# Kernel tuning notes

Hardware: AMD Instinct MI355X
Metric: run time of the kernel (lower is better)

The kernel has to match this reference:

```python
import jax, jax.numpy as jnp
import numpy as np

B = 512      # graphs per batch
NPG = 62     # nodes (electrodes) per graph
N = B * NPG  # total nodes per band
F_IN = 5     # node features
H = 8        # attention heads
C = 3        # num_classes (GATConv out channels, concat=False)
DEG = 16     # avg degree
EG = NPG * DEG
E = B * EG   # edges per band
NB = 5       # bands: delta, alpha, beta, theta, gamma
DE_DIM = 930 # 310*3


def setup_inputs() -> dict:
    key = jax.random.key(0)
    ks = jax.random.split(key, 24)
    x_bands = jax.random.normal(ks[0], (NB, N, F_IN), dtype=jnp.float32)
    # within-graph random edges: node ids in [g*62, g*62+62)
    base = (jnp.arange(B, dtype=jnp.int32) * NPG)[None, :, None]
    src = jax.random.randint(ks[1], (NB, B, EG), 0, NPG, dtype=jnp.int32) + base
    dst = jax.random.randint(ks[2], (NB, B, EG), 0, NPG, dtype=jnp.int32) + base
    edge_index_bands = jnp.stack([src.reshape(NB, E), dst.reshape(NB, E)], axis=1)  # [NB,2,E]
    batch = jnp.repeat(jnp.arange(B, dtype=jnp.int32), NPG)  # [N]
    de = jax.random.normal(ks[3], (B, NPG, 5, 3), dtype=jnp.float32)
    s = 0.3
    params = dict(
        bn_gamma=jnp.ones((NB, F_IN), jnp.float32),
        bn_beta=jnp.zeros((NB, F_IN), jnp.float32),
        W=jax.random.normal(ks[4], (NB, F_IN, H * C)) * s,
        att_src=jax.random.normal(ks[5], (NB, H, C)) * s,
        att_dst=jax.random.normal(ks[6], (NB, H, C)) * s,
        gat_bias=jax.random.normal(ks[7], (NB, C)) * 0.01,
        fg_W=jax.random.normal(ks[8], (NB * C, 64)) * s,
        fg_b=jnp.zeros((64,), jnp.float32),
        ln_g=jnp.ones((DE_DIM,), jnp.float32),
        ln_b=jnp.zeros((DE_DIM,), jnp.float32),
        q_W=jax.random.normal(ks[9], (DE_DIM, 64)) * 0.03,
        q_b=jnp.zeros((64,), jnp.float32),
        k_W=jax.random.normal(ks[10], (DE_DIM, 64)) * 0.03,
        k_b=jnp.zeros((64,), jnp.float32),
        v_W=jax.random.normal(ks[11], (DE_DIM, 64)) * 0.03,
        v_b=jnp.zeros((64,), jnp.float32),
        fa_W=jax.random.normal(ks[12], (128, C)) * s,
        fa_b=jnp.zeros((C,), jnp.float32),
    )
    return dict(x_bands=x_bands, edge_index_bands=edge_index_bands, batch=batch, de=de, **params)


def _gat_band(x, ei, g, b, Wb, a_src, a_dst, bias, batch):
    # BatchNorm1d (training-mode batch stats), eps=1e-5
    mu = x.mean(0)
    var = x.var(0)
    xn = (x - mu) * jax.lax.rsqrt(var + 1e-5) * g + b
    # GATConv(F_IN -> C, heads=H, concat=False) with self-loops
    xt = (xn @ Wb).reshape(N, H, C)                       # [N,H,C]
    al_s = (xt * a_src).sum(-1)                           # [N,H]
    al_d = (xt * a_dst).sum(-1)                           # [N,H]
    loop = jnp.arange(N, dtype=ei.dtype)
    src = jnp.concatenate([ei[0], loop])                  # [E+N]
    dst = jnp.concatenate([ei[1], loop])
    e = jax.nn.leaky_relu(al_s[src] + al_d[dst], 0.2)     # [E+N,H]
    m = jax.ops.segment_max(e, dst, num_segments=N)
    ex = jnp.exp(e - m[dst])
    denom = jax.ops.segment_sum(ex, dst, num_segments=N)  # [N,H]
    msg = ex[:, :, None] * xt[src]                        # [E+N,H,C]
    out = jax.ops.segment_sum(msg, dst, num_segments=N) / denom[:, :, None]
    out = out.mean(1) + bias                              # concat=False -> head mean
    out = jax.nn.elu(out)
    # global_mean_pool
    summed = jax.ops.segment_sum(out, batch, num_segments=B)
    cnt = jax.ops.segment_sum(jnp.ones((N,), out.dtype), batch, num_segments=B)
    return summed / cnt[:, None]                          # [B,C]


def reference(x_bands, edge_index_bands, batch, de, bn_gamma, bn_beta, W,
              att_src, att_dst, gat_bias, fg_W, fg_b, ln_g, ln_b,
              q_W, q_b, k_W, k_b, v_W, v_b, fa_W, fa_b):
    pooled = jax.vmap(_gat_band, in_axes=(0, 0, 0, 0, 0, 0, 0, 0, None))(
        x_bands, edge_index_bands, bn_gamma, bn_beta, W, att_src, att_dst, gat_bias, batch
    )  # [NB,B,C]
    x_concat = jnp.transpose(pooled, (1, 0, 2)).reshape(B, NB * C)  # [B,15]
    x_out = jax.nn.elu(x_concat @ fg_W + fg_b)                       # [B,64]
    # de branch: LayerNorm + self-attention
    de_f = de.reshape(B, DE_DIM)
    mu = de_f.mean(-1, keepdims=True)
    var = de_f.var(-1, keepdims=True)
    de_n = (de_f - mu) * jax.lax.rsqrt(var + 1e-5) * ln_g + ln_b
    Q = de_n @ q_W + q_b
    K = de_n @ k_W + k_b
    V = de_n @ v_W + v_b
    attn = jax.nn.softmax(Q @ K.T / jnp.sqrt(jnp.float32(64)), axis=-1)
    x_de = attn @ V                                                  # [B,64]
    # F.leaky_relu(x, negative_slope=1) is the identity
    out = jnp.concatenate([x_out, x_de], axis=1) @ fa_W + fa_b       # [B,3]
    return jax.nn.elu(out)
```

## Files before the change

### kernel.cpp

```cpp
#include <hip/hip_runtime.h>
#include <math.h>

#define NBANDS 5
#define BATCH  512
#define NPG    62
#define NTOT   (BATCH*NPG)
#define F_IN   5
#define NH     8
#define NC     3
#define HC     (NH*NC)
#define EG     (NPG*16)
#define ETOT   (BATCH*EG)
#define EPG    (EG+NPG)
#define DE_DIM 930
#define KS     5
#define KLEN   186

#define WS_BN     0
#define WS_LNS    512
#define WS_POOLED 1536
#define WS_Q      (WS_POOLED + NBANDS*BATCH*NC)
#define WS_KT     (WS_Q  + BATCH*64)
#define WS_V      (WS_KT + BATCH*64)
#define WS_PART   (WS_V  + BATCH*64)
#define WS_END    (WS_PART + 3*KS*BATCH*64)

__device__ __forceinline__ float eluf(float x) { return x > 0.f ? x : expm1f(x); }

__global__ __launch_bounds__(256) void stats_kernel(
    const float* __restrict__ x, const float* __restrict__ de,
    float* __restrict__ ws) {
    int bid = blockIdx.x;
    int tid = threadIdx.x;
    int w = tid >> 6, lane = tid & 63;
    if (bid < 40) {
        int band = bid >> 3, chunk = bid & 7;
        const int ROWS = NTOT / 8;
        int r0 = chunk * ROWS;
        const float* xb = x + (size_t)band * NTOT * F_IN;
        float s[F_IN] = {0,0,0,0,0}, q[F_IN] = {0,0,0,0,0};
        for (int r = r0 + tid; r < r0 + ROWS; r += 256) {
            const float* row = xb + (size_t)r * F_IN;
            #pragma unroll
            for (int f = 0; f < F_IN; ++f) { float v = row[f]; s[f] += v; q[f] += v * v; }
        }
        #pragma unroll
        for (int f = 0; f < F_IN; ++f) {
            for (int off = 32; off; off >>= 1) {
                s[f] += __shfl_down(s[f], off, 64);
                q[f] += __shfl_down(q[f], off, 64);
            }
        }
        __shared__ float part[4][10];
        if (lane == 0) {
            #pragma unroll
            for (int f = 0; f < F_IN; ++f) { part[w][f] = s[f]; part[w][5 + f] = q[f]; }
        }
        __syncthreads();
        if (tid < 10) {
            float t = part[0][tid] + part[1][tid] + part[2][tid] + part[3][tid];
            ws[WS_BN + (band * 8 + chunk) * 10 + tid] = t;
        }
    } else {
        int r = (bid - 40) * 4 + w;
        const float* row = de + (size_t)r * DE_DIM;
        float s1 = 0.f, s2 = 0.f;
        for (int i = lane; i < DE_DIM; i += 64) { float v = row[i]; s1 += v; s2 += v * v; }
        #pragma unroll
        for (int off = 32; off; off >>= 1) {
            s1 += __shfl_down(s1, off, 64);
            s2 += __shfl_down(s2, off, 64);
        }
        if (lane == 0) {
            float mu  = s1 * (1.0f / DE_DIM);
            float var = s2 * (1.0f / DE_DIM) - mu * mu;
            ws[WS_LNS + r * 2]     = mu;
            ws[WS_LNS + r * 2 + 1] = rsqrtf(var + 1e-5f);
        }
    }
}

__global__ __launch_bounds__(256) void gat_kernel(
    const float* __restrict__ x, const int* __restrict__ ei,
    const float* __restrict__ bn_g, const float* __restrict__ bn_b,
    const float* __restrict__ Wg, const float* __restrict__ attSg,
    const float* __restrict__ attDg, const float* __restrict__ biasg,
    const float* __restrict__ wsbn, float* __restrict__ pooled) {
    int g    = blockIdx.x;
    int band = blockIdx.y;
    __shared__ float Wl[F_IN * HC];
    __shared__ float attS[HC], attD[HC];
    __shared__ float bnsum[10];
    __shared__ float scale[F_IN], shift[F_IN];
    __shared__ float xns[NPG * F_IN];
    __shared__ float xt[NPG * HC];
    __shared__ float als[NPG * NH], ald[NPG * NH];
    __shared__ int   deg[NPG];
    __shared__ int   offs[NPG + 1];
    __shared__ int   cur[NPG];
    __shared__ int   csr[EPG];
    __shared__ float outd[NPG][NC];

    int tid = threadIdx.x;
    int lane = tid & 63;
    int nbase = g * NPG;

    if (tid < F_IN * HC) Wl[tid] = Wg[band * F_IN * HC + tid];
    if (tid >= 128 && tid < 128 + HC) attS[tid - 128] = attSg[band * HC + tid - 128];
    if (tid >= 160 && tid < 160 + HC) attD[tid - 160] = attDg[band * HC + tid - 160];
    if (tid < NPG) deg[tid] = 0;
    if (tid >= 192 && tid < 202) {
        int f = tid - 192;
        float t = 0.f;
        #pragma unroll
        for (int c = 0; c < 8; ++c) t += wsbn[(band * 8 + c) * 10 + f];
        bnsum[f] = t;
    }
    __syncthreads();

    const int* srcp = ei + (size_t)band * 2 * ETOT + (size_t)g * EG;
    const int* dstp = srcp + ETOT;

    for (int e = tid; e < EG; e += 256) atomicAdd(&deg[dstp[e] - nbase], 1);
    if (tid < F_IN) {
        float mu  = bnsum[tid] * (1.0f / NTOT);
        float var = bnsum[5 + tid] * (1.0f / NTOT) - mu * mu;
        float sc  = rsqrtf(var + 1e-5f) * bn_g[band * F_IN + tid];
        scale[tid] = sc;
        shift[tid] = bn_b[band * F_IN + tid] - mu * sc;
    }
    __syncthreads();

    {
        const float* xr = x + (size_t)band * NTOT * F_IN + (size_t)nbase * F_IN;
        for (int i = tid; i < NPG * F_IN; i += 256) {
            int f = i % F_IN;
            xns[i] = xr[i] * scale[f] + shift[f];
        }
    }
    if (tid >= 64 && tid < 128) {
        int l = lane;
        int dv = (l < NPG) ? deg[l] + 1 : 0;
        int sc = dv;
        #pragma unroll
        for (int off = 1; off < 64; off <<= 1) {
            int t = __shfl_up(sc, off, 64);
            if (l >= off) sc += t;
        }
        if (l < NPG) offs[l + 1] = sc;
        if (l == 0)  offs[0] = 0;
    }
    __syncthreads();

    for (int p = tid; p < NPG * HC; p += 256) {
        int n = p / HC, o = p - n * HC;
        float a = 0.f;
        #pragma unroll
        for (int f = 0; f < F_IN; ++f) a += xns[n * F_IN + f] * Wl[f * HC + o];
        xt[p] = a;
    }
    if (tid < NPG) { int o0 = offs[tid]; csr[o0] = tid; cur[tid] = o0 + 1; }
    __syncthreads();

    for (int p = tid; p < NPG * NH; p += 256) {
        int n = p >> 3, h = p & 7;
        float as = 0.f, ad = 0.f;
        #pragma unroll
        for (int c = 0; c < NC; ++c) {
            float v = xt[n * HC + h * NC + c];
            as += v * attS[h * NC + c];
            ad += v * attD[h * NC + c];
        }
        als[p] = as;
        ald[p] = ad;
    }
    for (int e = tid; e < EG; e += 256) {
        int ld = dstp[e] - nbase;
        int p = atomicAdd(&cur[ld], 1);
        csr[p] = srcp[e] - nbase;
    }
    __syncthreads();

    for (int p = tid; p < NPG * NH; p += 256) {
        int d = p >> 3, h = p & 7;
        int s0 = offs[d], s1 = offs[d + 1];
        float adv = ald[p];
        float den = 0.f, m0 = 0.f, m1 = 0.f, m2 = 0.f;
        for (int e = s0; e < s1; ++e) {
            int s = csr[e];
            float v = als[s * NH + h] + adv;
            v = v > 0.f ? v : 0.2f * v;
            float ex = __expf(v);
            den += ex;
            m0 += ex * xt[s * HC + h * NC + 0];
            m1 += ex * xt[s * HC + h * NC + 1];
            m2 += ex * xt[s * HC + h * NC + 2];
        }
        float rd = 1.0f / den;
        float o0 = m0 * rd, o1 = m1 * rd, o2 = m2 * rd;
        #pragma unroll
        for (int off = 1; off < 8; off <<= 1) {
            o0 += __shfl_xor(o0, off, 64);
            o1 += __shfl_xor(o1, off, 64);
            o2 += __shfl_xor(o2, off, 64);
        }
        if (h == 0) { outd[d][0] = o0; outd[d][1] = o1; outd[d][2] = o2; }
    }
    __syncthreads();

    float oc[NC] = {0.f, 0.f, 0.f};
    if (tid < NPG) {
        #pragma unroll
        for (int c = 0; c < NC; ++c)
            oc[c] = eluf(outd[tid][c] * (1.0f / NH) + biasg[band * NC + c]);
    }
    if (tid < 64) {
        #pragma unroll
        for (int c = 0; c < NC; ++c) {
            float v = oc[c];
            for (int off = 32; off; off >>= 1) v += __shfl_down(v, off, 64);
            if (tid == 0)
                pooled[((size_t)band * BATCH + g) * NC + c] = v * (1.0f / NPG);
        }
    }
}

__global__ __launch_bounds__(256) void qkv_partial(
    const float* __restrict__ de, const float* __restrict__ lns,
    const float* __restrict__ ln_g, const float* __restrict__ ln_b,
    const float* __restrict__ qW, const float* __restrict__ kW,
    const float* __restrict__ vW, float* __restrict__ part) {
    int rt = blockIdx.x;
    int m  = blockIdx.y;
    int ks = blockIdx.z;
    __shared__ float dl[4][KLEN];
    int tid = threadIdx.x, w = tid >> 6, col = tid & 63;
    for (int i = tid; i < 4 * KLEN; i += 256) {
        int rr = i / KLEN, ii = i - rr * KLEN;
        int row = rt * 4 + rr, gcol = ks * KLEN + ii;
        float mu = lns[row * 2], rstd = lns[row * 2 + 1];
        dl[rr][ii] = (de[(size_t)row * DE_DIM + gcol] - mu) * rstd * ln_g[gcol] + ln_b[gcol];
    }
    __syncthreads();
    const float* Wm = ((m == 0) ? qW : (m == 1) ? kW : vW) + (size_t)ks * KLEN * 64;
    float a[6] = {0, 0, 0, 0, 0, 0};
    for (int i = 0; i < KLEN; i += 6) {
        #pragma unroll
        for (int j = 0; j < 6; ++j)
            a[j] += dl[w][i + j] * Wm[(size_t)(i + j) * 64 + col];
    }
    float acc = ((a[0] + a[1]) + (a[2] + a[3])) + (a[4] + a[5]);
    part[(((size_t)m * KS + ks) * BATCH + rt * 4 + w) * 64 + col] = acc;
}

__global__ __launch_bounds__(256) void qkv_reduce(
    const float* __restrict__ part,
    const float* __restrict__ qb, const float* __restrict__ kb,
    const float* __restrict__ vb,
    float* __restrict__ Q, float* __restrict__ KT, float* __restrict__ V) {
    int idx = blockIdx.x * 256 + threadIdx.x;
    int m  = idx >> 15;
    int local = idx & 32767;
    if (m == 1) {
        int row = local & 511, col = local >> 9;
        float s = 0.f;
        #pragma unroll
        for (int ks = 0; ks < KS; ++ks)
            s += part[(((size_t)KS + ks) << 15) + (row << 6) + col];
        KT[local] = s + kb[col];
    } else {
        int col = local & 63;
        float s = 0.f;
        #pragma unroll
        for (int ks = 0; ks < KS; ++ks)
            s += part[(((size_t)m * KS + ks) << 15) + local];
        s += (m == 0) ? qb[col] : vb[col];
        ((m == 0) ? Q : V)[local] = s;
    }
}

__global__ __launch_bounds__(256) void qkv_fused_fb(
    const float* __restrict__ de, const float* __restrict__ ln_g,
    const float* __restrict__ ln_b,
    const float* __restrict__ qW, const float* __restrict__ qb,
    const float* __restrict__ kW, const float* __restrict__ kb,
    const float* __restrict__ vW, const float* __restrict__ vb,
    float* __restrict__ Q, float* __restrict__ KT, float* __restrict__ V) {
    int r0 = blockIdx.x * 4;
    int m  = blockIdx.y;
    __shared__ float dn[4][DE_DIM];
    int tid  = threadIdx.x;
    int w    = tid >> 6, lane = tid & 63;
    const float* row = de + (size_t)(r0 + w) * DE_DIM;
    float s1 = 0.f, s2 = 0.f;
    for (int i = lane; i < DE_DIM; i += 64) {
        float v = row[i]; dn[w][i] = v; s1 += v; s2 += v * v;
    }
    #pragma unroll
    for (int off = 32; off; off >>= 1) {
        s1 += __shfl_down(s1, off, 64);
        s2 += __shfl_down(s2, off, 64);
    }
    float mu   = __shfl(s1, 0, 64) * (1.0f / DE_DIM);
    float var  = __shfl(s2, 0, 64) * (1.0f / DE_DIM) - mu * mu;
    float rstd = rsqrtf(var + 1e-5f);
    for (int i = lane; i < DE_DIM; i += 64)
        dn[w][i] = (dn[w][i] - mu) * rstd * ln_g[i] + ln_b[i];
    __syncthreads();
    const float* Wm = (m == 0) ? qW : (m == 1) ? kW : vW;
    const float* bm = (m == 0) ? qb : (m == 1) ? kb : vb;
    float a[10];
    #pragma unroll
    for (int j = 0; j < 10; ++j) a[j] = 0.f;
    for (int i = 0; i < DE_DIM; i += 10) {
        #pragma unroll
        for (int j = 0; j < 10; ++j)
            a[j] += dn[w][i + j] * Wm[(size_t)(i + j) * 64 + lane];
    }
    float acc = (((a[0] + a[1]) + (a[2] + a[3])) + ((a[4] + a[5]) + (a[6] + a[7])))
              + (a[8] + a[9]) + bm[lane];
    int r = r0 + w;
    if (m == 1) KT[lane * BATCH + r] = acc;
    else ((m == 0) ? Q : V)[(size_t)r * 64 + lane] = acc;
}

__global__ __launch_bounds__(256) void attn_final(
    const float* __restrict__ Q, const float* __restrict__ KT,
    const float* __restrict__ V, const float* __restrict__ pooled,
    const float* __restrict__ fgW, const float* __restrict__ fgb,
    const float* __restrict__ faW, const float* __restrict__ fab,
    float* __restrict__ out) {
    int b = blockIdx.x;
    int tid = threadIdx.x;
    __shared__ float qrow[64];
    __shared__ float p[BATCH];
    __shared__ float red[8];
    __shared__ float pv[4][64];
    __shared__ float xde[64], xout[64];
    if (tid < 64) qrow[tid] = Q[(size_t)b * 64 + tid];
    __syncthreads();

    float a0 = 0.f, a1 = 0.f, b0 = 0.f, b1 = 0.f;
    #pragma unroll 8
    for (int i = 0; i < 64; i += 2) {
        float q0 = qrow[i], q1 = qrow[i + 1];
        a0 += q0 * KT[(size_t)i * BATCH + tid];
        a1 += q1 * KT[(size_t)(i + 1) * BATCH + tid];
        b0 += q0 * KT[(size_t)i * BATCH + tid + 256];
        b1 += q1 * KT[(size_t)(i + 1) * BATCH + tid + 256];
    }
    float sj0 = (a0 + a1) * 0.125f, sj1 = (b0 + b1) * 0.125f;

    float mx = fmaxf(sj0, sj1);
    for (int off = 32; off; off >>= 1) mx = fmaxf(mx, __shfl_down(mx, off, 64));
    if ((tid & 63) == 0) red[tid >> 6] = mx;
    __syncthreads();
    mx = fmaxf(fmaxf(red[0], red[1]), fmaxf(red[2], red[3]));
    float e0 = __expf(sj0 - mx), e1 = __expf(sj1 - mx);
    p[tid] = e0; p[tid + 256] = e1;
    float s = e0 + e1;
    for (int off = 32; off; off >>= 1) s += __shfl_down(s, off, 64);
    if ((tid & 63) == 0) red[4 + (tid >> 6)] = s;
    __syncthreads();
    float denom = red[4] + red[5] + red[6] + red[7];

    int o = tid & 63, cq = tid >> 6;
    float acc = 0.f;
    #pragma unroll 4
    for (int j = cq * 128; j < cq * 128 + 128; ++j)
        acc += p[j] * V[(size_t)j * 64 + o];
    pv[cq][o] = acc;
    __syncthreads();
    if (tid < 64)
        xde[tid] = (pv[0][tid] + pv[1][tid] + pv[2][tid] + pv[3][tid]) / denom;
    if (tid >= 64 && tid < 128) {
        int oo = tid - 64;
        float a = fgb[oo];
        #pragma unroll
        for (int j = 0; j < NBANDS * NC; ++j) {
            int band = j / NC, c = j % NC;
            a += pooled[((size_t)band * BATCH + b) * NC + c] * fgW[j * 64 + oo];
        }
        xout[oo] = eluf(a);
    }
    __syncthreads();
    if (tid < NC) {
        float a = fab[tid];
        for (int i = 0; i < 64; ++i) a += xout[i] * faW[i * NC + tid];
        for (int i = 0; i < 64; ++i) a += xde[i] * faW[(64 + i) * NC + tid];
        out[(size_t)b * NC + tid] = eluf(a);
    }
}

extern "C" void kernel_launch(void* const* d_in, const int* in_sizes, int n_in,
                              void* d_out, int out_size, void* d_ws, size_t ws_size,
                              hipStream_t stream) {
    const float* x     = (const float*)d_in[0];
    const int*   ei    = (const int*)  d_in[1];
    const float* de    = (const float*)d_in[3];
    const float* bn_g  = (const float*)d_in[4];
    const float* bn_b  = (const float*)d_in[5];
    const float* W     = (const float*)d_in[6];
    const float* attS  = (const float*)d_in[7];
    const float* attD  = (const float*)d_in[8];
    const float* gbias = (const float*)d_in[9];
    const float* fgW   = (const float*)d_in[10];
    const float* fgb   = (const float*)d_in[11];
    const float* ln_g  = (const float*)d_in[12];
    const float* ln_b  = (const float*)d_in[13];
    const float* qW    = (const float*)d_in[14];
    const float* qb    = (const float*)d_in[15];
    const float* kW    = (const float*)d_in[16];
    const float* kb    = (const float*)d_in[17];
    const float* vW    = (const float*)d_in[18];
    const float* vb    = (const float*)d_in[19];
    const float* faW   = (const float*)d_in[20];
    const float* fab   = (const float*)d_in[21];
    float* ws  = (float*)d_ws;
    float* out = (float*)d_out;

    stats_kernel<<<168, 256, 0, stream>>>(x, de, ws);
    gat_kernel<<<dim3(BATCH, NBANDS), 256, 0, stream>>>(
        x, ei, bn_g, bn_b, W, attS, attD, gbias, ws + WS_BN, ws + WS_POOLED);

    if (ws_size >= (size_t)WS_END * sizeof(float)) {
        qkv_partial<<<dim3(BATCH / 4, 3, KS), 256, 0, stream>>>(
            de, ws + WS_LNS, ln_g, ln_b, qW, kW, vW, ws + WS_PART);
        qkv_reduce<<<(3 * BATCH * 64) / 256, 256, 0, stream>>>(
            ws + WS_PART, qb, kb, vb, ws + WS_Q, ws + WS_KT, ws + WS_V);
    } else {
        qkv_fused_fb<<<dim3(BATCH / 4, 3), 256, 0, stream>>>(
            de, ln_g, ln_b, qW, qb, kW, kb, vW, vb,
            ws + WS_Q, ws + WS_KT, ws + WS_V);
    }
    attn_final<<<BATCH, 256, 0, stream>>>(ws + WS_Q, ws + WS_KT, ws + WS_V,
                                          ws + WS_POOLED, fgW, fgb, faW, fab, out);
}
```

Before: 74.95 us.

## Merge GAT and QKV-partial launches into one kernel and pack attention data

Folds the per-graph GAT kernel and the QKV partial GEMM into a single launch that dispatches on block index, with the two roles sharing one shared-memory buffer. This removes a kernel launch and lets the independent GAT and QKV work overlap on the GPU. GAT node features and the source attention logit are packed into a float4 so the edge loop does one LDS read per edge, and the projection is fused with the attention logit computation. The BN stats loop now reads x as float4 groups. Sharing shared memory sizes it to the larger GAT struct for every block, which may lower occupancy for the QKV blocks.

```diff
diff --git a/kernel.cpp b/kernel.cpp
--- a/kernel.cpp
+++ b/kernel.cpp
@@ -16,6 +16,10 @@
 #define KS     5
 #define KLEN   186
 
+#define GAT_BLOCKS  (BATCH*NBANDS)
+#define QKVP_BLOCKS (128*3*KS)
+#define MID_BLOCKS  (GAT_BLOCKS + QKVP_BLOCKS)
+
 #define WS_BN     0
 #define WS_LNS    512
 #define WS_POOLED 1536
@@ -35,14 +39,20 @@
     int w = tid >> 6, lane = tid & 63;
     if (bid < 40) {
         int band = bid >> 3, chunk = bid & 7;
-        const int ROWS = NTOT / 8;
-        int r0 = chunk * ROWS;
-        const float* xb = x + (size_t)band * NTOT * F_IN;
+        const int G4 = NTOT / 8 / 4;
+        const float4* xb4 =
+            (const float4*)(x + (size_t)band * NTOT * F_IN) + (size_t)chunk * G4 * 5;
         float s[F_IN] = {0,0,0,0,0}, q[F_IN] = {0,0,0,0,0};
-        for (int r = r0 + tid; r < r0 + ROWS; r += 256) {
-            const float* row = xb + (size_t)r * F_IN;
-            #pragma unroll
-            for (int f = 0; f < F_IN; ++f) { float v = row[f]; s[f] += v; q[f] += v * v; }
+        for (int gi = tid; gi < G4; gi += 256) {
+            const float4* p4 = xb4 + (size_t)gi * 5;
+            float vv[20];
+            *(float4*)&vv[0]  = p4[0];
+            *(float4*)&vv[4]  = p4[1];
+            *(float4*)&vv[8]  = p4[2];
+            *(float4*)&vv[12] = p4[3];
+            *(float4*)&vv[16] = p4[4];
+            #pragma unroll
+            for (int i = 0; i < 20; ++i) { float v = vv[i]; s[i % 5] += v; q[i % 5] += v * v; }
         }
         #pragma unroll
         for (int f = 0; f < F_IN; ++f) {
@@ -80,177 +90,188 @@
     }
 }
 
-__global__ __launch_bounds__(256) void gat_kernel(
+struct GatShared {
+    float  Wl[F_IN * HC];
+    float  attS[HC], attD[HC];
+    float  bnsum[10];
+    float  scale[F_IN], shift[F_IN];
+    float  xns[NPG * F_IN];
+    float4 xt4[NPG * NH];
+    float  ald[NPG * NH];
+    int    deg[NPG];
+    int    offs[NPG + 1];
+    int    cur[NPG];
+    int    csr[EPG];
+    float  outd[NPG][NC];
+};
+struct QkvShared { float dl[4][KLEN]; };
+
+__global__ __launch_bounds__(256) void mid_kernel(
     const float* __restrict__ x, const int* __restrict__ ei,
     const float* __restrict__ bn_g, const float* __restrict__ bn_b,
     const float* __restrict__ Wg, const float* __restrict__ attSg,
     const float* __restrict__ attDg, const float* __restrict__ biasg,
-    const float* __restrict__ wsbn, float* __restrict__ pooled) {
-    int g    = blockIdx.x;
-    int band = blockIdx.y;
-    __shared__ float Wl[F_IN * HC];
-    __shared__ float attS[HC], attD[HC];
-    __shared__ float bnsum[10];
-    __shared__ float scale[F_IN], shift[F_IN];
-    __shared__ float xns[NPG * F_IN];
-    __shared__ float xt[NPG * HC];
-    __shared__ float als[NPG * NH], ald[NPG * NH];
-    __shared__ int   deg[NPG];
-    __shared__ int   offs[NPG + 1];
-    __shared__ int   cur[NPG];
-    __shared__ int   csr[EPG];
-    __shared__ float outd[NPG][NC];
-
+    const float* __restrict__ de, const float* __restrict__ ln_g,
+    const float* __restrict__ ln_b,
+    const float* __restrict__ qW, const float* __restrict__ kW,
+    const float* __restrict__ vW,
+    const float* __restrict__ ws_in, float* __restrict__ ws_out) {
+    __shared__ __align__(16) unsigned char smem[sizeof(GatShared)];
+    int bid = blockIdx.x;
     int tid = threadIdx.x;
-    int lane = tid & 63;
-    int nbase = g * NPG;
-
-    if (tid < F_IN * HC) Wl[tid] = Wg[band * F_IN * HC + tid];
-    if (tid >= 128 && tid < 128 + HC) attS[tid - 128] = attSg[band * HC + tid - 128];
-    if (tid >= 160 && tid < 160 + HC) attD[tid - 160] = attDg[band * HC + tid - 160];
-    if (tid < NPG) deg[tid] = 0;
-    if (tid >= 192 && tid < 202) {
-        int f = tid - 192;
-        float t = 0.f;
-        #pragma unroll
-        for (int c = 0; c < 8; ++c) t += wsbn[(band * 8 + c) * 10 + f];
-        bnsum[f] = t;
-    }
-    __syncthreads();
-
-    const int* srcp = ei + (size_t)band * 2 * ETOT + (size_t)g * EG;
-    const int* dstp = srcp + ETOT;
-
-    for (int e = tid; e < EG; e += 256) atomicAdd(&deg[dstp[e] - nbase], 1);
-    if (tid < F_IN) {
-        float mu  = bnsum[tid] * (1.0f / NTOT);
-        float var = bnsum[5 + tid] * (1.0f / NTOT) - mu * mu;
-        float sc  = rsqrtf(var + 1e-5f) * bn_g[band * F_IN + tid];
-        scale[tid] = sc;
-        shift[tid] = bn_b[band * F_IN + tid] - mu * sc;
-    }
-    __syncthreads();
-
-    {
-        const float* xr = x + (size_t)band * NTOT * F_IN + (size_t)nbase * F_IN;
-        for (int i = tid; i < NPG * F_IN; i += 256) {
-            int f = i % F_IN;
-            xns[i] = xr[i] * scale[f] + shift[f];
-        }
-    }
-    if (tid >= 64 && tid < 128) {
-        int l = lane;
-        int dv = (l < NPG) ? deg[l] + 1 : 0;
-        int sc = dv;
-        #pragma unroll
-        for (int off = 1; off < 64; off <<= 1) {
-            int t = __shfl_up(sc, off, 64);
-            if (l >= off) sc += t;
-        }
-        if (l < NPG) offs[l + 1] = sc;
-        if (l == 0)  offs[0] = 0;
-    }
-    __syncthreads();
-
-    for (int p = tid; p < NPG * HC; p += 256) {
-        int n = p / HC, o = p - n * HC;
-        float a = 0.f;
-        #pragma unroll
-        for (int f = 0; f < F_IN; ++f) a += xns[n * F_IN + f] * Wl[f * HC + o];
-        xt[p] = a;
-    }
-    if (tid < NPG) { int o0 = offs[tid]; csr[o0] = tid; cur[tid] = o0 + 1; }
-    __syncthreads();
-
-    for (int p = tid; p < NPG * NH; p += 256) {
-        int n = p >> 3, h = p & 7;
-        float as = 0.f, ad = 0.f;
-        #pragma unroll
-        for (int c = 0; c < NC; ++c) {
-            float v = xt[n * HC + h * NC + c];
-            as += v * attS[h * NC + c];
-            ad += v * attD[h * NC + c];
-        }
-        als[p] = as;
-        ald[p] = ad;
-    }
-    for (int e = tid; e < EG; e += 256) {
-        int ld = dstp[e] - nbase;
-        int p = atomicAdd(&cur[ld], 1);
-        csr[p] = srcp[e] - nbase;
-    }
-    __syncthreads();
-
-    for (int p = tid; p < NPG * NH; p += 256) {
-        int d = p >> 3, h = p & 7;
-        int s0 = offs[d], s1 = offs[d + 1];
-        float adv = ald[p];
-        float den = 0.f, m0 = 0.f, m1 = 0.f, m2 = 0.f;
-        for (int e = s0; e < s1; ++e) {
-            int s = csr[e];
-            float v = als[s * NH + h] + adv;
-            v = v > 0.f ? v : 0.2f * v;
-            float ex = __expf(v);
-            den += ex;
-            m0 += ex * xt[s * HC + h * NC + 0];
-            m1 += ex * xt[s * HC + h * NC + 1];
-            m2 += ex * xt[s * HC + h * NC + 2];
-        }
-        float rd = 1.0f / den;
-        float o0 = m0 * rd, o1 = m1 * rd, o2 = m2 * rd;
-        #pragma unroll
-        for (int off = 1; off < 8; off <<= 1) {
-            o0 += __shfl_xor(o0, off, 64);
-            o1 += __shfl_xor(o1, off, 64);
-            o2 += __shfl_xor(o2, off, 64);
-        }
-        if (h == 0) { outd[d][0] = o0; outd[d][1] = o1; outd[d][2] = o2; }
-    }
-    __syncthreads();
-
-    float oc[NC] = {0.f, 0.f, 0.f};
-    if (tid < NPG) {
-        #pragma unroll
-        for (int c = 0; c < NC; ++c)
-            oc[c] = eluf(outd[tid][c] * (1.0f / NH) + biasg[band * NC + c]);
-    }
-    if (tid < 64) {
-        #pragma unroll
-        for (int c = 0; c < NC; ++c) {
-            float v = oc[c];
-            for (int off = 32; off; off >>= 1) v += __shfl_down(v, off, 64);
-            if (tid == 0)
-                pooled[((size_t)band * BATCH + g) * NC + c] = v * (1.0f / NPG);
-        }
-    }
-}
-
-__global__ __launch_bounds__(256) void qkv_partial(
-    const float* __restrict__ de, const float* __restrict__ lns,
-    const float* __restrict__ ln_g, const float* __restrict__ ln_b,
-    const float* __restrict__ qW, const float* __restrict__ kW,
-    const float* __restrict__ vW, float* __restrict__ part) {
-    int rt = blockIdx.x;
-    int m  = blockIdx.y;
-    int ks = blockIdx.z;
-    __shared__ float dl[4][KLEN];
-    int tid = threadIdx.x, w = tid >> 6, col = tid & 63;
-    for (int i = tid; i < 4 * KLEN; i += 256) {
-        int rr = i / KLEN, ii = i - rr * KLEN;
-        int row = rt * 4 + rr, gcol = ks * KLEN + ii;
-        float mu = lns[row * 2], rstd = lns[row * 2 + 1];
-        dl[rr][ii] = (de[(size_t)row * DE_DIM + gcol] - mu) * rstd * ln_g[gcol] + ln_b[gcol];
-    }
-    __syncthreads();
-    const float* Wm = ((m == 0) ? qW : (m == 1) ? kW : vW) + (size_t)ks * KLEN * 64;
-    float a[6] = {0, 0, 0, 0, 0, 0};
-    for (int i = 0; i < KLEN; i += 6) {
-        #pragma unroll
-        for (int j = 0; j < 6; ++j)
-            a[j] += dl[w][i + j] * Wm[(size_t)(i + j) * 64 + col];
-    }
-    float acc = ((a[0] + a[1]) + (a[2] + a[3])) + (a[4] + a[5]);
-    part[(((size_t)m * KS + ks) * BATCH + rt * 4 + w) * 64 + col] = acc;
+
+    if (bid < GAT_BLOCKS) {
+        GatShared& S = *reinterpret_cast<GatShared*>(smem);
+        int g    = bid & 511;
+        int band = bid >> 9;
+        int lane = tid & 63;
+        int nbase = g * NPG;
+        const float* wsbn = ws_in + WS_BN;
+        float* pooled = ws_out + WS_POOLED;
+
+        if (tid < F_IN * HC) S.Wl[tid] = Wg[band * F_IN * HC + tid];
+        if (tid >= 128 && tid < 128 + HC) S.attS[tid - 128] = attSg[band * HC + tid - 128];
+        if (tid >= 160 && tid < 160 + HC) S.attD[tid - 160] = attDg[band * HC + tid - 160];
+        if (tid < NPG) S.deg[tid] = 0;
+        if (tid >= 192 && tid < 202) {
+            int f = tid - 192;
+            float t = 0.f;
+            #pragma unroll
+            for (int c = 0; c < 8; ++c) t += wsbn[(band * 8 + c) * 10 + f];
+            S.bnsum[f] = t;
+        }
+        __syncthreads();
+
+        const int* srcp = ei + (size_t)band * 2 * ETOT + (size_t)g * EG;
+        const int* dstp = srcp + ETOT;
+
+        for (int e = tid; e < EG; e += 256) atomicAdd(&S.deg[dstp[e] - nbase], 1);
+        if (tid < F_IN) {
+            float mu  = S.bnsum[tid] * (1.0f / NTOT);
+            float var = S.bnsum[5 + tid] * (1.0f / NTOT) - mu * mu;
+            float sc  = rsqrtf(var + 1e-5f) * bn_g[band * F_IN + tid];
+            S.scale[tid] = sc;
+            S.shift[tid] = bn_b[band * F_IN + tid] - mu * sc;
+        }
+        __syncthreads();
+
+        {
+            const float* xr = x + (size_t)band * NTOT * F_IN + (size_t)nbase * F_IN;
+            for (int i = tid; i < NPG * F_IN; i += 256) {
+                int f = i % F_IN;
+                S.xns[i] = xr[i] * S.scale[f] + S.shift[f];
+            }
+        }
+        if (tid >= 64 && tid < 128) {
+            int l = lane;
+            int dv = (l < NPG) ? S.deg[l] + 1 : 0;
+            int sc = dv;
+            #pragma unroll
+            for (int off = 1; off < 64; off <<= 1) {
+                int t = __shfl_up(sc, off, 64);
+                if (l >= off) sc += t;
+            }
+            if (l < NPG) S.offs[l + 1] = sc;
+            if (l == 0)  S.offs[0] = 0;
+        }
+        __syncthreads();
+
+        for (int p = tid; p < NPG * NH; p += 256) {
+            int n = p >> 3, h = p & 7;
+            float c0 = 0.f, c1 = 0.f, c2 = 0.f;
+            #pragma unroll
+            for (int f = 0; f < F_IN; ++f) {
+                float xv = S.xns[n * F_IN + f];
+                c0 += xv * S.Wl[f * HC + h * NC + 0];
+                c1 += xv * S.Wl[f * HC + h * NC + 1];
+                c2 += xv * S.Wl[f * HC + h * NC + 2];
+            }
+            float as = c0 * S.attS[h * NC] + c1 * S.attS[h * NC + 1] + c2 * S.attS[h * NC + 2];
+            float ad = c0 * S.attD[h * NC] + c1 * S.attD[h * NC + 1] + c2 * S.attD[h * NC + 2];
+            S.xt4[p] = make_float4(c0, c1, c2, as);
+            S.ald[p] = ad;
+        }
+        if (tid < NPG) { int o0 = S.offs[tid]; S.csr[o0] = tid; S.cur[tid] = o0 + 1; }
+        __syncthreads();
+
+        for (int e = tid; e < EG; e += 256) {
+            int ld = dstp[e] - nbase;
+            int p = atomicAdd(&S.cur[ld], 1);
+            S.csr[p] = srcp[e] - nbase;
+        }
+        __syncthreads();
+
+        for (int p = tid; p < NPG * NH; p += 256) {
+            int d = p >> 3, h = p & 7;
+            int s0 = S.offs[d], s1 = S.offs[d + 1];
+            float adv = S.ald[p];
+            float den = 0.f, m0 = 0.f, m1 = 0.f, m2 = 0.f;
+            for (int e = s0; e < s1; ++e) {
+                int s = S.csr[e];
+                float4 t = S.xt4[(s << 3) + h];
+                float v = t.w + adv;
+                v = v > 0.f ? v : 0.2f * v;
+                float ex = __expf(v);
+                den += ex;
+                m0 += ex * t.x;
+                m1 += ex * t.y;
+                m2 += ex * t.z;
+            }
+            float rd = 1.0f / den;
+            float o0 = m0 * rd, o1 = m1 * rd, o2 = m2 * rd;
+            #pragma unroll
+            for (int off = 1; off < 8; off <<= 1) {
+                o0 += __shfl_xor(o0, off, 64);
+                o1 += __shfl_xor(o1, off, 64);
+                o2 += __shfl_xor(o2, off, 64);
+            }
+            if (h == 0) { S.outd[d][0] = o0; S.outd[d][1] = o1; S.outd[d][2] = o2; }
+        }
+        __syncthreads();
+
+        float oc[NC] = {0.f, 0.f, 0.f};
+        if (tid < NPG) {
+            #pragma unroll
+            for (int c = 0; c < NC; ++c)
+                oc[c] = eluf(S.outd[tid][c] * (1.0f / NH) + biasg[band * NC + c]);
+        }
+        if (tid < 64) {
+            #pragma unroll
+            for (int c = 0; c < NC; ++c) {
+                float v = oc[c];
+                for (int off = 32; off; off >>= 1) v += __shfl_down(v, off, 64);
+                if (tid == 0)
+                    pooled[((size_t)band * BATCH + g) * NC + c] = v * (1.0f / NPG);
+            }
+        }
+    } else {
+        QkvShared& P = *reinterpret_cast<QkvShared*>(smem);
+        int q  = bid - GAT_BLOCKS;
+        int ks = q / 384;
+        int r3 = q - ks * 384;
+        int m  = r3 >> 7;
+        int rt = r3 & 127;
+        const float* lns = ws_in + WS_LNS;
+        float* part = ws_out + WS_PART;
+
+        int w = tid >> 6, col = tid & 63;
+        for (int i = tid; i < 4 * KLEN; i += 256) {
+            int rr = i / KLEN, ii = i - rr * KLEN;
+            int row = rt * 4 + rr, gcol = ks * KLEN + ii;
+            float mu = lns[row * 2], rstd = lns[row * 2 + 1];
+            P.dl[rr][ii] = (de[(size_t)row * DE_DIM + gcol] - mu) * rstd * ln_g[gcol] + ln_b[gcol];
+        }
+        __syncthreads();
+        const float* Wm = ((m == 0) ? qW : (m == 1) ? kW : vW) + (size_t)ks * KLEN * 64;
+        float a[6] = {0, 0, 0, 0, 0, 0};
+        for (int i = 0; i < KLEN; i += 6) {
+            #pragma unroll
+            for (int j = 0; j < 6; ++j)
+                a[j] += P.dl[w][i + j] * Wm[(size_t)(i + j) * 64 + col];
+        }
+        float acc = ((a[0] + a[1]) + (a[2] + a[3])) + (a[4] + a[5]);
+        part[(((size_t)m * KS + ks) * BATCH + rt * 4 + w) * 64 + col] = acc;
+    }
 }
 
 __global__ __launch_bounds__(256) void qkv_reduce(
@@ -420,15 +441,17 @@
     float* out = (float*)d_out;
 
     stats_kernel<<<168, 256, 0, stream>>>(x, de, ws);
-    gat_kernel<<<dim3(BATCH, NBANDS), 256, 0, stream>>>(
-        x, ei, bn_g, bn_b, W, attS, attD, gbias, ws + WS_BN, ws + WS_POOLED);
 
     if (ws_size >= (size_t)WS_END * sizeof(float)) {
-        qkv_partial<<<dim3(BATCH / 4, 3, KS), 256, 0, stream>>>(
-            de, ws + WS_LNS, ln_g, ln_b, qW, kW, vW, ws + WS_PART);
+        mid_kernel<<<MID_BLOCKS, 256, 0, stream>>>(
+            x, ei, bn_g, bn_b, W, attS, attD, gbias,
+            de, ln_g, ln_b, qW, kW, vW, ws, ws);
         qkv_reduce<<<(3 * BATCH * 64) / 256, 256, 0, stream>>>(
             ws + WS_PART, qb, kb, vb, ws + WS_Q, ws + WS_KT, ws + WS_V);
     } else {
+        mid_kernel<<<GAT_BLOCKS, 256, 0, stream>>>(
+            x, ei, bn_g, bn_b, W, attS, attD, gbias,
+            de, ln_g, ln_b, qW, kW, vW, ws, ws);
         qkv_fused_fb<<<dim3(BATCH / 4, 3), 256, 0, stream>>>(
             de, ln_g, ln_b, qW, qb, kW, kb, vW, vb,
             ws + WS_Q, ws + WS_KT, ws + WS_V);
```

Measured after the change: 78.16 us. +4.3%, slower.

## Pack per-head features and source logits into padded float4 LDS, vectorize stats loads

Applied to the files above, without the earlier changes.

The node projection and the attention-logit computation are merged into one pass per (node, head), which removes one block-wide barrier. Each head's three features and its source logit are stored together as a padded float4 (stride 9), so the edge aggregation loop reads one vector from LDS instead of four scalars. The BatchNorm stats kernel now loads x as groups of five float4s covering four rows each, replacing strided scalar loads. The cost is more LDS for xt and a 20-element register array in the stats loop.

```diff
diff --git a/kernel.cpp b/kernel.cpp
--- a/kernel.cpp
+++ b/kernel.cpp
@@ -15,6 +15,7 @@
 #define DE_DIM 930
 #define KS     5
 #define KLEN   186
+#define XTS    9
 
 #define WS_BN     0
 #define WS_LNS    512
@@ -35,14 +36,20 @@
     int w = tid >> 6, lane = tid & 63;
     if (bid < 40) {
         int band = bid >> 3, chunk = bid & 7;
-        const int ROWS = NTOT / 8;
-        int r0 = chunk * ROWS;
-        const float* xb = x + (size_t)band * NTOT * F_IN;
+        const int G4 = NTOT / 8 / 4;
+        const float4* xb4 =
+            (const float4*)(x + (size_t)band * NTOT * F_IN) + (size_t)chunk * G4 * 5;
         float s[F_IN] = {0,0,0,0,0}, q[F_IN] = {0,0,0,0,0};
-        for (int r = r0 + tid; r < r0 + ROWS; r += 256) {
-            const float* row = xb + (size_t)r * F_IN;
+        for (int gi = tid; gi < G4; gi += 256) {
+            const float4* p4 = xb4 + (size_t)gi * 5;
+            float vv[20];
+            *(float4*)&vv[0]  = p4[0];
+            *(float4*)&vv[4]  = p4[1];
+            *(float4*)&vv[8]  = p4[2];
+            *(float4*)&vv[12] = p4[3];
+            *(float4*)&vv[16] = p4[4];
             #pragma unroll
-            for (int f = 0; f < F_IN; ++f) { float v = row[f]; s[f] += v; q[f] += v * v; }
+            for (int i = 0; i < 20; ++i) { float v = vv[i]; s[i % 5] += v; q[i % 5] += v * v; }
         }
         #pragma unroll
         for (int f = 0; f < F_IN; ++f) {
@@ -88,18 +95,18 @@
     const float* __restrict__ wsbn, float* __restrict__ pooled) {
     int g    = blockIdx.x;
     int band = blockIdx.y;
-    __shared__ float Wl[F_IN * HC];
-    __shared__ float attS[HC], attD[HC];
-    __shared__ float bnsum[10];
-    __shared__ float scale[F_IN], shift[F_IN];
-    __shared__ float xns[NPG * F_IN];
-    __shared__ float xt[NPG * HC];
-    __shared__ float als[NPG * NH], ald[NPG * NH];
-    __shared__ int   deg[NPG];
-    __shared__ int   offs[NPG + 1];
-    __shared__ int   cur[NPG];
-    __shared__ int   csr[EPG];
-    __shared__ float outd[NPG][NC];
+    __shared__ float  Wl[F_IN * HC];
+    __shared__ float  attS[HC], attD[HC];
+    __shared__ float  bnsum[10];
+    __shared__ float  scale[F_IN], shift[F_IN];
+    __shared__ float  xns[NPG * F_IN];
+    __shared__ float4 xt4[NPG * XTS];
+    __shared__ float  ald[NPG * NH];
+    __shared__ int    deg[NPG];
+    __shared__ int    offs[NPG + 1];
+    __shared__ int    cur[NPG];
+    __shared__ int    csr[EPG];
+    __shared__ float  outd[NPG][NC];
 
     int tid = threadIdx.x;
     int lane = tid & 63;
@@ -152,28 +159,24 @@
     }
     __syncthreads();
 
-    for (int p = tid; p < NPG * HC; p += 256) {
-        int n = p / HC, o = p - n * HC;
-        float a = 0.f;
-        #pragma unroll
-        for (int f = 0; f < F_IN; ++f) a += xns[n * F_IN + f] * Wl[f * HC + o];
-        xt[p] = a;
-    }
-    if (tid < NPG) { int o0 = offs[tid]; csr[o0] = tid; cur[tid] = o0 + 1; }
-    __syncthreads();
-
     for (int p = tid; p < NPG * NH; p += 256) {
         int n = p >> 3, h = p & 7;
-        float as = 0.f, ad = 0.f;
-        #pragma unroll
-        for (int c = 0; c < NC; ++c) {
-            float v = xt[n * HC + h * NC + c];
-            as += v * attS[h * NC + c];
-            ad += v * attD[h * NC + c];
-        }
-        als[p] = as;
+        float c0 = 0.f, c1 = 0.f, c2 = 0.f;
+        #pragma unroll
+        for (int f = 0; f < F_IN; ++f) {
+            float xv = xns[n * F_IN + f];
+            c0 += xv * Wl[f * HC + h * NC + 0];
+            c1 += xv * Wl[f * HC + h * NC + 1];
+            c2 += xv * Wl[f * HC + h * NC + 2];
+        }
+        float as = c0 * attS[h * NC] + c1 * attS[h * NC + 1] + c2 * attS[h * NC + 2];
+        float ad = c0 * attD[h * NC] + c1 * attD[h * NC + 1] + c2 * attD[h * NC + 2];
+        xt4[n * XTS + h] = make_float4(c0, c1, c2, as);
         ald[p] = ad;
     }
+    if (tid < NPG) { int o0 = offs[tid]; csr[o0] = tid; cur[tid] = o0 + 1; }
+    __syncthreads();
+
     for (int e = tid; e < EG; e += 256) {
         int ld = dstp[e] - nbase;
         int p = atomicAdd(&cur[ld], 1);
@@ -188,13 +191,14 @@
         float den = 0.f, m0 = 0.f, m1 = 0.f, m2 = 0.f;
         for (int e = s0; e < s1; ++e) {
             int s = csr[e];
-            float v = als[s * NH + h] + adv;
+            float4 t = xt4[s * XTS + h];
+            float v = t.w + adv;
             v = v > 0.f ? v : 0.2f * v;
             float ex = __expf(v);
             den += ex;
-            m0 += ex * xt[s * HC + h * NC + 0];
-            m1 += ex * xt[s * HC + h * NC + 1];
-            m2 += ex * xt[s * HC + h * NC + 2];
+            m0 += ex * t.x;
+            m1 += ex * t.y;
+            m2 += ex * t.z;
         }
         float rd = 1.0f / den;
         float o0 = m0 * rd, o1 = m1 * rd, o2 = m2 * rd;
```

After: 69.73 us. 7.0% less time.
